# Kernel optimization log

Hardware: AMD Instinct MI355X
Metric: run time of the kernel (lower is better)

The kernel has to match this reference:

```python
import jax, jax.numpy as jnp
from jax import lax
import numpy as np

B, T, L, D, TOPK, KC = 8, 4096, 256, 128, 8, 9  # KC = ctx conv kernel size


def setup_inputs() -> dict:
    key = jax.random.key(0)
    ks = jax.random.split(key, 9)
    s = 0.05
    return {
        "x": jax.random.normal(ks[0], (B, T), jnp.float32),
        "lag_embed": jax.random.normal(ks[1], (L + 1, D), jnp.float32) * s,  # nn.Embedding(L+1, d)
        "val_w": jax.random.normal(ks[2], (D, 1), jnp.float32) * s,          # nn.Linear(1, d) weight
        "val_b": jnp.zeros((D,), jnp.float32),
        "conv_w": jax.random.normal(ks[3], (D, 1, KC), jnp.float32) * s,     # Conv1d(1, d, 9) weight (O,I,K)
        "conv_b": jnp.zeros((D,), jnp.float32),
        "ctx_w": jax.random.normal(ks[4], (D, D), jnp.float32) * s,          # ctx_proj
        "ctx_b": jnp.zeros((D,), jnp.float32),
        "wq": jax.random.normal(ks[5], (D, D), jnp.float32) * s,             # Wq (no bias)
        "wk": jax.random.normal(ks[6], (D, D), jnp.float32) * s,             # Wk (no bias)
        "bias_w": jax.random.normal(ks[7], (1, D), jnp.float32) * s,         # bias_head
        "bias_b": jnp.zeros((1,), jnp.float32),
    }


def _lag_bank(x, Lv):
    # Xlags[b, t, l] = x[b, t-(l+1)], left-padded with zeros (per docstring/intended math)
    Bv, Tv = x.shape
    pads = jnp.pad(x, ((0, 0), (Lv, 0)))
    idx = Lv - 1 + jnp.arange(Tv)[:, None] - jnp.arange(Lv)[None, :]  # (T, L)
    return pads[:, idx]  # (B, T, L)


def reference(x, lag_embed, val_w, val_b, conv_w, conv_b, ctx_w, ctx_b, wq, wk, bias_w, bias_b):
    Xlags = _lag_bank(x, L)  # (B, T, L)

    # Causal context conv: left-pad 8 zeros, Conv1d(1, D, 9, padding=0)
    xp = jnp.pad(x, ((0, 0), (KC - 1, 0)))[:, None, :]  # (B, 1, T+8)
    ctx = lax.conv_general_dilated(xp, conv_w, (1,), 'VALID',
                                   dimension_numbers=('NCH', 'OIH', 'NCH'))
    ctx = ctx + conv_b[None, :, None]           # (B, D, T)
    ctx = jnp.transpose(ctx, (0, 2, 1))         # (B, T, D)
    ctx = ctx @ ctx_w.T + ctx_b                 # ctx_proj

    q = ctx @ wq.T                              # (B, T, D)
    # score = <q, Wk Hlag> = <Wk^T q, Hlag>; Hlag = Xlags*val_w + (val_b + lag_embed[1:L+1])
    # is rank-1 in the value -> never materialize the (B,T,L,D) tensor.
    qk = q @ wk                                 # (B, T, D) = Wk^T q
    base = val_b[None, :] + lag_embed[1:L + 1]  # (L, D)
    logits = Xlags * (qk @ val_w[:, 0])[:, :, None] + qk @ base.T  # (B, T, L)

    # top-k sparsification (ties are measure-zero with continuous inputs)
    kth = lax.top_k(logits, TOPK)[0][..., -1:]
    masked = jnp.where(logits >= kth, logits, -jnp.inf)
    w = jax.nn.softmax(masked, axis=-1)         # (B, T, L)

    mu = jnp.sum(w * Xlags, axis=-1) + (ctx @ bias_w.T)[..., 0] + bias_b[0]  # (B, T)
    return mu, w
```

## Files before the change

kernel.cpp:

```cpp
#include <hip/hip_runtime.h>
#include <math.h>

#define D   128
#define LQ  256
#define KCQ 9
#define BQ  8
#define TQ  4096
#define RISK_DELTA 2e-5f
#define WCAP 16384

__global__ void pk1(const float* __restrict__ wk, const float* __restrict__ wq,
                    const float* __restrict__ ctx_w, const float* __restrict__ bias_w,
                    const float* __restrict__ conv_w, const float* __restrict__ val_b,
                    const float* __restrict__ lag_embed,
                    double* __restrict__ T2, double* __restrict__ u, int* __restrict__ wcnt,
                    float* __restrict__ ctx_wT, float* __restrict__ wqT,
                    float* __restrict__ conv_wT, float* __restrict__ baseT) {
    int tid = threadIdx.x;
    int bid = blockIdx.x;
    if (bid < D) {
        int d = bid;
        if (tid < D) {
            double acc = 0.0;
            for (int j = 0; j < D; ++j)
                acc += (double)wk[j * D + d] * (double)wq[j * D + tid];
            T2[d * D + tid] = acc;
            ctx_wT[d * D + tid] = ctx_w[tid * D + d];
            wqT[d * D + tid]    = wq[tid * D + d];
            if (d < KCQ) conv_wT[d * D + tid] = conv_w[tid * KCQ + d];
        }
        baseT[d * LQ + tid] = __fadd_rn(val_b[d], lag_embed[(size_t)(tid + 1) * D + d]);
    } else if (bid == D) {
        if (tid < D) {
            double acc = 0.0;
            for (int dd = 0; dd < D; ++dd)
                acc += (double)bias_w[dd] * (double)ctx_w[dd * D + tid];
            u[tid] = acc;
        }
    } else {
        if (tid == 0) *wcnt = 0;
    }
}

__global__ void pk2(const double* __restrict__ T2, const float* __restrict__ ctx_w,
                    const float* __restrict__ conv_w, const float* __restrict__ conv_b,
                    const float* __restrict__ ctx_b,
                    double* __restrict__ g, double* __restrict__ c1) {
    __shared__ double row[D];
    int d = blockIdx.x, e = threadIdx.x;
    double acc = 0.0;
    for (int j = 0; j < D; ++j)
        acc += T2[d * D + j] * (double)ctx_w[j * D + e];
    row[e] = acc;
    __syncthreads();
    if (e < KCQ) {
        double a = 0.0;
        for (int q = 0; q < D; ++q) a += row[q] * (double)conv_w[q * KCQ + e];
        g[e * D + d] = a;
    } else if (e == KCQ) {
        double a = 0.0;
        for (int q = 0; q < D; ++q) a += row[q] * (double)conv_b[q];
        for (int q = 0; q < D; ++q) a += T2[d * D + q] * (double)ctx_b[q];
        c1[d] = a;
    }
}

__global__ void pk3(const float* __restrict__ lag_embed, const float* __restrict__ val_b,
                    const float* __restrict__ val_w, const float* __restrict__ conv_w,
                    const float* __restrict__ conv_b, const float* __restrict__ ctx_b,
                    const float* __restrict__ bias_w, const float* __restrict__ bias_b,
                    const double* __restrict__ g, const double* __restrict__ c1,
                    const double* __restrict__ u,
                    double* __restrict__ gbT, double* __restrict__ cbv, double* __restrict__ cst) {
    int tid = threadIdx.x;
    if (blockIdx.x < LQ) {
        __shared__ double bl[D];
        int l = blockIdx.x;
        bl[tid] = (double)val_b[tid] + (double)lag_embed[(l + 1) * D + tid];
        __syncthreads();
        if (tid < KCQ) {
            double a = 0.0;
            for (int q = 0; q < D; ++q) a += bl[q] * g[tid * D + q];
            gbT[tid * LQ + l] = a;
        } else if (tid == KCQ) {
            double a = 0.0;
            for (int q = 0; q < D; ++q) a += bl[q] * c1[q];
            cbv[l] = a;
        }
    } else {
        if (tid < KCQ) {
            double a = 0.0, a2 = 0.0;
            for (int q = 0; q < D; ++q) a  += g[tid * D + q] * (double)val_w[q];
            for (int q = 0; q < D; ++q) a2 += u[q] * (double)conv_w[q * KCQ + tid];
            cst[tid]      = a;
            cst[10 + tid] = a2;
        } else if (tid == KCQ) {
            double a = 0.0, a2 = 0.0;
            for (int q = 0; q < D; ++q) a  += c1[q] * (double)val_w[q];
            for (int q = 0; q < D; ++q) a2 += u[q] * (double)conv_b[q];
            for (int q = 0; q < D; ++q) a2 += (double)bias_w[q] * (double)ctx_b[q];
            cst[9]  = a;
            cst[19] = a2 + (double)bias_b[0];
        }
    }
}

__global__ __launch_bounds__(256, 4) void lag_main(
    const float* __restrict__ x, const double* __restrict__ gbT,
    const double* __restrict__ cbv, const double* __restrict__ cst,
    float* __restrict__ muOut, float* __restrict__ wOut,
    int* __restrict__ wcnt, int* __restrict__ wlist) {
    __shared__ float sgb[KCQ * LQ];
    __shared__ float scb[LQ];
    __shared__ float sc[20];
    int tid = threadIdx.x;
    #pragma unroll
    for (int i = 0; i < KCQ; ++i) sgb[i * LQ + tid] = (float)gbT[i * LQ + tid];
    scb[tid] = (float)cbv[tid];
    if (tid < 20) sc[tid] = (float)cst[tid];
    __syncthreads();

    int wave = tid >> 6, lane = tid & 63;
    int row = blockIdx.x * 4 + wave;
    int b = row >> 12;
    int t = row & (TQ - 1);
    const float* xb = x + b * TQ;

    float xw[KCQ];
    #pragma unroll
    for (int k = 0; k < KCQ; ++k) {
        int idx = t - 8 + k;
        xw[k] = (idx >= 0) ? xb[idx] : 0.f;
    }
    float s = sc[9], bias = sc[19];
    #pragma unroll
    for (int k = 0; k < KCQ; ++k) {
        s    = fmaf(sc[k],      xw[k], s);
        bias = fmaf(sc[10 + k], xw[k], bias);
    }

    int l0 = lane * 4;
    float xlag[4];
    #pragma unroll
    for (int i = 0; i < 4; ++i) {
        int idx = t - 1 - (l0 + i);
        xlag[i] = (idx >= 0) ? xb[idx] : 0.f;
    }

    float4 cb4 = *reinterpret_cast<const float4*>(&scb[l0]);
    float lg[4] = {cb4.x, cb4.y, cb4.z, cb4.w};
    #pragma unroll
    for (int k = 0; k < KCQ; ++k) {
        float4 g4 = *reinterpret_cast<const float4*>(&sgb[k * LQ + l0]);
        lg[0] = fmaf(g4.x, xw[k], lg[0]);
        lg[1] = fmaf(g4.y, xw[k], lg[1]);
        lg[2] = fmaf(g4.z, xw[k], lg[2]);
        lg[3] = fmaf(g4.w, xw[k], lg[3]);
    }
    #pragma unroll
    for (int i = 0; i < 4; ++i) lg[i] = fmaf(xlag[i], s, lg[i]);

    const float NEG_INF = -__builtin_inff();
    float wl0 = lg[0], wl1 = lg[1], wl2 = lg[2], wl3 = lg[3];
    float mx = 0.f, thr = 0.f, v9 = 0.f;
    #pragma unroll
    for (int it = 0; it < 9; ++it) {
        float lm = fmaxf(fmaxf(wl0, wl1), fmaxf(wl2, wl3));
        float m = lm;
        #pragma unroll
        for (int off = 32; off >= 1; off >>= 1)
            m = fmaxf(m, __shfl_xor(m, off, 64));
        if (it == 0) mx = m;
        if (it == 7) thr = m;
        if (it == 8) v9 = m;
        if (it < 8) {
            unsigned long long ball = __ballot(lm == m);
            int leader = __ffsll(ball) - 1;
            if (lane == leader) {
                if (wl0 == m)      wl0 = NEG_INF;
                else if (wl1 == m) wl1 = NEG_INF;
                else if (wl2 == m) wl2 = NEG_INF;
                else               wl3 = NEG_INF;
            }
        }
    }

    if ((thr - v9) < RISK_DELTA) {
        if (lane == 0) {
            int pos = atomicAdd(wcnt, 1);
            if (pos < WCAP) wlist[pos] = row;
        }
        return;
    }

    float p[4], psum = 0.f, pmu = 0.f;
    #pragma unroll
    for (int j = 0; j < 4; ++j) {
        p[j] = (lg[j] >= thr) ? __expf(lg[j] - mx) : 0.f;
        psum += p[j];
        pmu = fmaf(p[j], xlag[j], pmu);
    }
    #pragma unroll
    for (int off = 32; off >= 1; off >>= 1) {
        psum += __shfl_xor(psum, off, 64);
        pmu  += __shfl_xor(pmu,  off, 64);
    }
    float inv = 1.f / psum;
    float4 wo = make_float4(p[0] * inv, p[1] * inv, p[2] * inv, p[3] * inv);
    *reinterpret_cast<float4*>(&wOut[(size_t)row * LQ + l0]) = wo;
    if (lane == 0) muOut[row] = fmaf(pmu, inv, bias);
}

__global__ __launch_bounds__(256) void fixer(
    const float* __restrict__ x, const float* __restrict__ wk,
    const float* __restrict__ val_w, const float* __restrict__ conv_b,
    const float* __restrict__ ctx_b, const float* __restrict__ bias_w,
    const float* __restrict__ bias_b,
    const float* __restrict__ ctx_wT, const float* __restrict__ wqT,
    const float* __restrict__ conv_wT, const float* __restrict__ baseT,
    const int* __restrict__ wcnt, const int* __restrict__ wlist,
    float* __restrict__ muOut, float* __restrict__ wOut) {
    __shared__ float sxw[8][KCQ];
    __shared__ float sctxc[8][D];
    __shared__ float sctxp[8][D];
    __shared__ float sq[8][D];
    __shared__ float sqk[8][D];
    __shared__ float ssv[8];
    __shared__ float sbd[8];
    __shared__ float slog[8][LQ];
    __shared__ int   srow[8];

    int cnt = *wcnt;
    if (cnt > WCAP) cnt = WCAP;
    int ngroups = (cnt + 7) >> 3;
    int tid = threadIdx.x;

    for (int gi = blockIdx.x; gi < ngroups; gi += gridDim.x) {
        if (tid < 8) {
            int idx = gi * 8 + tid;
            if (idx >= cnt) idx = cnt - 1;
            srow[tid] = wlist[idx];
        }
        __syncthreads();
        if (tid < 8 * KCQ) {
            int g = tid / KCQ, k = tid % KCQ;
            int row = srow[g]; int b = row >> 12, t = row & (TQ - 1);
            int ii = t - 8 + k;
            sxw[g][k] = (ii >= 0) ? x[b * TQ + ii] : 0.f;
        }
        __syncthreads();

        {
            int d = tid & (D - 1), gh = tid >> 7;
            float cw[KCQ];
            #pragma unroll
            for (int k = 0; k < KCQ; ++k) cw[k] = conv_wT[k * D + d];
            #pragma unroll 1
            for (int g = gh * 4; g < gh * 4 + 4; ++g) {
                float a = 0.f;
                #pragma unroll
                for (int k = 0; k < KCQ; ++k)
                    a = fmaf(cw[k], sxw[g][k], a);
                sctxc[g][d] = __fadd_rn(a, conv_b[d]);
            }
        }
        __syncthreads();

        {
            int e = tid & (D - 1), gh = tid >> 7, g0 = gh * 4;
            float a0 = 0.f, a1 = 0.f, a2 = 0.f, a3 = 0.f;
            float wv0[16], wv1[16];
            #pragma unroll
            for (int u = 0; u < 16; ++u) wv0[u] = ctx_wT[u * D + e];
            #pragma unroll 1
            for (int d2 = 0; d2 < D; d2 += 32) {
                #pragma unroll
                for (int u = 0; u < 16; ++u) wv1[u] = ctx_wT[(d2 + 16 + u) * D + e];
                #pragma unroll
                for (int u = 0; u < 16; ++u) {
                    a0 = fmaf(wv0[u], sctxc[g0 + 0][d2 + u], a0);
                    a1 = fmaf(wv0[u], sctxc[g0 + 1][d2 + u], a1);
                    a2 = fmaf(wv0[u], sctxc[g0 + 2][d2 + u], a2);
                    a3 = fmaf(wv0[u], sctxc[g0 + 3][d2 + u], a3);
                }
                if (d2 + 32 < D) {
                    #pragma unroll
                    for (int u = 0; u < 16; ++u) wv0[u] = ctx_wT[(d2 + 32 + u) * D + e];
                }
                #pragma unroll
                for (int u = 0; u < 16; ++u) {
                    a0 = fmaf(wv1[u], sctxc[g0 + 0][d2 + 16 + u], a0);
                    a1 = fmaf(wv1[u], sctxc[g0 + 1][d2 + 16 + u], a1);
                    a2 = fmaf(wv1[u], sctxc[g0 + 2][d2 + 16 + u], a2);
                    a3 = fmaf(wv1[u], sctxc[g0 + 3][d2 + 16 + u], a3);
                }
            }
            float cb = ctx_b[e];
            sctxp[g0 + 0][e] = __fadd_rn(a0, cb);
            sctxp[g0 + 1][e] = __fadd_rn(a1, cb);
            sctxp[g0 + 2][e] = __fadd_rn(a2, cb);
            sctxp[g0 + 3][e] = __fadd_rn(a3, cb);
        }
        __syncthreads();

        {
            int a = tid & (D - 1), gh = tid >> 7, g0 = gh * 4;
            float a0 = 0.f, a1 = 0.f, a2 = 0.f, a3 = 0.f;
            float wv0[16], wv1[16];
            #pragma unroll
            for (int u = 0; u < 16; ++u) wv0[u] = wqT[u * D + a];
            #pragma unroll 1
            for (int e2 = 0; e2 < D; e2 += 32) {
                #pragma unroll
                for (int u = 0; u < 16; ++u) wv1[u] = wqT[(e2 + 16 + u) * D + a];
                #pragma unroll
                for (int u = 0; u < 16; ++u) {
                    a0 = fmaf(wv0[u], sctxp[g0 + 0][e2 + u], a0);
                    a1 = fmaf(wv0[u], sctxp[g0 + 1][e2 + u], a1);
                    a2 = fmaf(wv0[u], sctxp[g0 + 2][e2 + u], a2);
                    a3 = fmaf(wv0[u], sctxp[g0 + 3][e2 + u], a3);
                }
                if (e2 + 32 < D) {
                    #pragma unroll
                    for (int u = 0; u < 16; ++u) wv0[u] = wqT[(e2 + 32 + u) * D + a];
                }
                #pragma unroll
                for (int u = 0; u < 16; ++u) {
                    a0 = fmaf(wv1[u], sctxp[g0 + 0][e2 + 16 + u], a0);
                    a1 = fmaf(wv1[u], sctxp[g0 + 1][e2 + 16 + u], a1);
                    a2 = fmaf(wv1[u], sctxp[g0 + 2][e2 + 16 + u], a2);
                    a3 = fmaf(wv1[u], sctxp[g0 + 3][e2 + 16 + u], a3);
                }
            }
            sq[g0 + 0][a] = a0;
            sq[g0 + 1][a] = a1;
            sq[g0 + 2][a] = a2;
            sq[g0 + 3][a] = a3;
        }
        __syncthreads();

        {
            int d = tid & (D - 1), gh = tid >> 7, g0 = gh * 4;
            float a0 = 0.f, a1 = 0.f, a2 = 0.f, a3 = 0.f;
            float wv0[16], wv1[16];
            #pragma unroll
            for (int u = 0; u < 16; ++u) wv0[u] = wk[u * D + d];
            #pragma unroll 1
            for (int a2i = 0; a2i < D; a2i += 32) {
                #pragma unroll
                for (int u = 0; u < 16; ++u) wv1[u] = wk[(a2i + 16 + u) * D + d];
                #pragma unroll
                for (int u = 0; u < 16; ++u) {
                    a0 = fmaf(wv0[u], sq[g0 + 0][a2i + u], a0);
                    a1 = fmaf(wv0[u], sq[g0 + 1][a2i + u], a1);
                    a2 = fmaf(wv0[u], sq[g0 + 2][a2i + u], a2);
                    a3 = fmaf(wv0[u], sq[g0 + 3][a2i + u], a3);
                }
                if (a2i + 32 < D) {
                    #pragma unroll
                    for (int u = 0; u < 16; ++u) wv0[u] = wk[(a2i + 32 + u) * D + d];
                }
                #pragma unroll
                for (int u = 0; u < 16; ++u) {
                    a0 = fmaf(wv1[u], sq[g0 + 0][a2i + 16 + u], a0);
                    a1 = fmaf(wv1[u], sq[g0 + 1][a2i + 16 + u], a1);
                    a2 = fmaf(wv1[u], sq[g0 + 2][a2i + 16 + u], a2);
                    a3 = fmaf(wv1[u], sq[g0 + 3][a2i + 16 + u], a3);
                }
            }
            sqk[g0 + 0][d] = a0;
            sqk[g0 + 1][d] = a1;
            sqk[g0 + 2][d] = a2;
            sqk[g0 + 3][d] = a3;
        }
        __syncthreads();

        if (tid < 8) {
            int g = tid;
            float a = 0.f;
            #pragma unroll 1
            for (int d2 = 0; d2 < D; d2 += 16) {
                float vv[16];
                #pragma unroll
                for (int u = 0; u < 16; ++u) vv[u] = val_w[d2 + u];
                #pragma unroll
                for (int u = 0; u < 16; ++u) a = fmaf(sqk[g][d2 + u], vv[u], a);
            }
            ssv[g] = a;
        } else if (tid < 16) {
            int g = tid - 8;
            float a = 0.f;
            #pragma unroll 1
            for (int e2 = 0; e2 < D; e2 += 16) {
                float vv[16];
                #pragma unroll
                for (int u = 0; u < 16; ++u) vv[u] = bias_w[e2 + u];
                #pragma unroll
                for (int u = 0; u < 16; ++u) a = fmaf(sctxp[g][e2 + u], vv[u], a);
            }
            sbd[g] = a;
        }
        __syncthreads();

        {
            int l = tid;
            float c0 = 0.f, c1a = 0.f, c2 = 0.f, c3 = 0.f, c4 = 0.f, c5 = 0.f, c6 = 0.f, c7 = 0.f;
            float bd0[16], bd1[16];
            #pragma unroll
            for (int u = 0; u < 16; ++u) bd0[u] = baseT[u * LQ + l];
            #pragma unroll 1
            for (int d2 = 0; d2 < D; d2 += 32) {
                #pragma unroll
                for (int u = 0; u < 16; ++u) bd1[u] = baseT[(d2 + 16 + u) * LQ + l];
                #pragma unroll
                for (int u = 0; u < 16; ++u) {
                    c0 = fmaf(bd0[u], sqk[0][d2 + u], c0);
                    c1a = fmaf(bd0[u], sqk[1][d2 + u], c1a);
                    c2 = fmaf(bd0[u], sqk[2][d2 + u], c2);
                    c3 = fmaf(bd0[u], sqk[3][d2 + u], c3);
                    c4 = fmaf(bd0[u], sqk[4][d2 + u], c4);
                    c5 = fmaf(bd0[u], sqk[5][d2 + u], c5);
                    c6 = fmaf(bd0[u], sqk[6][d2 + u], c6);
                    c7 = fmaf(bd0[u], sqk[7][d2 + u], c7);
                }
                if (d2 + 32 < D) {
                    #pragma unroll
                    for (int u = 0; u < 16; ++u) bd0[u] = baseT[(d2 + 32 + u) * LQ + l];
                }
                #pragma unroll
                for (int u = 0; u < 16; ++u) {
                    c0 = fmaf(bd1[u], sqk[0][d2 + 16 + u], c0);
                    c1a = fmaf(bd1[u], sqk[1][d2 + 16 + u], c1a);
                    c2 = fmaf(bd1[u], sqk[2][d2 + 16 + u], c2);
                    c3 = fmaf(bd1[u], sqk[3][d2 + 16 + u], c3);
                    c4 = fmaf(bd1[u], sqk[4][d2 + 16 + u], c4);
                    c5 = fmaf(bd1[u], sqk[5][d2 + 16 + u], c5);
                    c6 = fmaf(bd1[u], sqk[6][d2 + 16 + u], c6);
                    c7 = fmaf(bd1[u], sqk[7][d2 + 16 + u], c7);
                }
            }
            float accs[8] = {c0, c1a, c2, c3, c4, c5, c6, c7};
            #pragma unroll
            for (int g = 0; g < 8; ++g) {
                int row = srow[g]; int b = row >> 12, t = row & (TQ - 1);
                int ii = t - 1 - l;
                float xl = (ii >= 0) ? x[b * TQ + ii] : 0.f;
                slog[g][l] = __fadd_rn(__fmul_rn(xl, ssv[g]), accs[g]);
            }
        }
        __syncthreads();

        {
            int wave = tid >> 6, lane = tid & 63;
            #pragma unroll 1
            for (int gg = wave * 2; gg < wave * 2 + 2; ++gg) {
                float lv0 = slog[gg][lane], lv1 = slog[gg][lane + 64];
                float lv2 = slog[gg][lane + 128], lv3 = slog[gg][lane + 192];
                const float NEG_INF = -__builtin_inff();
                float w0 = lv0, w1 = lv1, w2 = lv2, w3 = lv3;
                float mx = 0.f, thr = 0.f;
                #pragma unroll
                for (int it = 0; it < 8; ++it) {
                    float lm = fmaxf(fmaxf(w0, w1), fmaxf(w2, w3));
                    float m = lm;
                    #pragma unroll
                    for (int off = 32; off >= 1; off >>= 1)
                        m = fmaxf(m, __shfl_xor(m, off, 64));
                    if (it == 0) mx = m;
                    thr = m;
                    if (it < 7) {
                        unsigned long long ball = __ballot(lm == m);
                        int leader = __ffsll(ball) - 1;
                        if (lane == leader) {
                            if (w0 == m)      w0 = NEG_INF;
                            else if (w1 == m) w1 = NEG_INF;
                            else if (w2 == m) w2 = NEG_INF;
                            else              w3 = NEG_INF;
                        }
                    }
                }
                int row = srow[gg]; int b = row >> 12, t = row & (TQ - 1);
                float p[4], xlg[4];
                double ps = 0.0;
                float lvs[4] = {lv0, lv1, lv2, lv3};
                #pragma unroll
                for (int j = 0; j < 4; ++j) {
                    int l = lane + 64 * j;
                    int ii = t - 1 - l;
                    xlg[j] = (ii >= 0) ? x[b * TQ + ii] : 0.f;
                    p[j] = (lvs[j] >= thr) ? (float)exp((double)__fsub_rn(lvs[j], mx)) : 0.f;
                    ps += (double)p[j];
                }
                #pragma unroll
                for (int off = 32; off >= 1; off >>= 1)
                    ps += __shfl_xor(ps, off, 64);
                float psf = (float)ps;
                double mud = 0.0;
                #pragma unroll
                for (int j = 0; j < 4; ++j) {
                    float wv = __fdiv_rn(p[j], psf);
                    wOut[(size_t)row * LQ + lane + 64 * j] = wv;
                    mud += (double)__fmul_rn(wv, xlg[j]);
                }
                #pragma unroll
                for (int off = 32; off >= 1; off >>= 1)
                    mud += __shfl_xor(mud, off, 64);
                if (lane == 0) {
                    float m1 = (float)mud;
                    m1 = __fadd_rn(m1, sbd[gg]);
                    m1 = __fadd_rn(m1, bias_b[0]);
                    muOut[row] = m1;
                }
            }
        }
        __syncthreads();
    }
}

extern "C" void kernel_launch(void* const* d_in, const int* in_sizes, int n_in,
                              void* d_out, int out_size, void* d_ws, size_t ws_size,
                              hipStream_t stream) {
    const float* x         = (const float*)d_in[0];
    const float* lag_embed = (const float*)d_in[1];
    const float* val_w     = (const float*)d_in[2];
    const float* val_b     = (const float*)d_in[3];
    const float* conv_w    = (const float*)d_in[4];
    const float* conv_b    = (const float*)d_in[5];
    const float* ctx_w     = (const float*)d_in[6];
    const float* ctx_b     = (const float*)d_in[7];
    const float* wq        = (const float*)d_in[8];
    const float* wk        = (const float*)d_in[9];
    const float* bias_w    = (const float*)d_in[10];
    const float* bias_b    = (const float*)d_in[11];

    char* wsb = (char*)d_ws;
    double* T2  = (double*)wsb;
    double* g   = T2 + 16384;
    double* u   = g + 1152;
    double* c1  = u + 128;
    double* gbT = c1 + 128;
    double* cbv = gbT + 2304;
    double* cst = cbv + 256;
    int* wcnt  = (int*)(wsb + 163840);
    int* wlist = wcnt + 1;
    float* ctx_wT  = (float*)(wsb + 229504);
    float* wqT     = ctx_wT + 16384;
    float* conv_wT = wqT + 16384;
    float* baseT   = conv_wT + 1152;

    float* muOut = (float*)d_out;
    float* wOut  = muOut + BQ * TQ;

    hipLaunchKernelGGL(pk1, dim3(D + 2), dim3(256), 0, stream,
                       wk, wq, ctx_w, bias_w, conv_w, val_b, lag_embed,
                       T2, u, wcnt, ctx_wT, wqT, conv_wT, baseT);
    hipLaunchKernelGGL(pk2, dim3(D), dim3(D), 0, stream, T2, ctx_w, conv_w, conv_b, ctx_b, g, c1);
    hipLaunchKernelGGL(pk3, dim3(LQ + 1), dim3(D), 0, stream,
                       lag_embed, val_b, val_w, conv_w, conv_b, ctx_b, bias_w, bias_b,
                       g, c1, u, gbT, cbv, cst);
    hipLaunchKernelGGL(lag_main, dim3(BQ * TQ / 4), dim3(256), 0, stream,
                       x, gbT, cbv, cst, muOut, wOut, wcnt, wlist);
    hipLaunchKernelGGL(fixer, dim3(256), dim3(256), 0, stream,
                       x, wk, val_w, conv_b, ctx_b, bias_w, bias_b,
                       ctx_wT, wqT, conv_wT, baseT, wcnt, wlist, muOut, wOut);
}
```

Before: 101.0 us.

## Store precomputed tables as float, raise occupancy, simplify top-k removal

The precompute kernel now writes its gbT/cbv/cst tables directly as float, so the main kernel no longer loads doubles and converts them when staging into shared memory. The main kernel's launch bounds rise from 4 to 8 blocks per SM to allow more concurrency. The top-k extraction loop replaces the ballot/leader single-element removal with a branch-free per-lane select. That select removes every element equal to the max, which differs from the old code only on exact ties. The fixer's bias dot product also drops its 16-wide register staging for a plain loop.

New measurement: 106.6 us. 5.5% more time.

```diff
diff --git a/kernel.cpp b/kernel.cpp
--- a/kernel.cpp
+++ b/kernel.cpp
@@ -71,7 +71,7 @@
                     const float* __restrict__ bias_w, const float* __restrict__ bias_b,
                     const double* __restrict__ g, const double* __restrict__ c1,
                     const double* __restrict__ u,
-                    double* __restrict__ gbT, double* __restrict__ cbv, double* __restrict__ cst) {
+                    float* __restrict__ gbTf, float* __restrict__ cbvf, float* __restrict__ cstf) {
     int tid = threadIdx.x;
     if (blockIdx.x < LQ) {
         __shared__ double bl[D];
@@ -81,33 +81,33 @@
         if (tid < KCQ) {
             double a = 0.0;
             for (int q = 0; q < D; ++q) a += bl[q] * g[tid * D + q];
-            gbT[tid * LQ + l] = a;
+            gbTf[tid * LQ + l] = (float)a;
         } else if (tid == KCQ) {
             double a = 0.0;
             for (int q = 0; q < D; ++q) a += bl[q] * c1[q];
-            cbv[l] = a;
+            cbvf[l] = (float)a;
         }
     } else {
         if (tid < KCQ) {
             double a = 0.0, a2 = 0.0;
             for (int q = 0; q < D; ++q) a  += g[tid * D + q] * (double)val_w[q];
             for (int q = 0; q < D; ++q) a2 += u[q] * (double)conv_w[q * KCQ + tid];
-            cst[tid]      = a;
-            cst[10 + tid] = a2;
+            cstf[tid]      = (float)a;
+            cstf[10 + tid] = (float)a2;
         } else if (tid == KCQ) {
             double a = 0.0, a2 = 0.0;
             for (int q = 0; q < D; ++q) a  += c1[q] * (double)val_w[q];
             for (int q = 0; q < D; ++q) a2 += u[q] * (double)conv_b[q];
             for (int q = 0; q < D; ++q) a2 += (double)bias_w[q] * (double)ctx_b[q];
-            cst[9]  = a;
-            cst[19] = a2 + (double)bias_b[0];
+            cstf[9]  = (float)a;
+            cstf[19] = (float)(a2 + (double)bias_b[0]);
         }
     }
 }
 
-__global__ __launch_bounds__(256, 4) void lag_main(
-    const float* __restrict__ x, const double* __restrict__ gbT,
-    const double* __restrict__ cbv, const double* __restrict__ cst,
+__global__ __launch_bounds__(256, 8) void lag_main(
+    const float* __restrict__ x, const float* __restrict__ gbTf,
+    const float* __restrict__ cbvf, const float* __restrict__ cstf,
     float* __restrict__ muOut, float* __restrict__ wOut,
     int* __restrict__ wcnt, int* __restrict__ wlist) {
     __shared__ float sgb[KCQ * LQ];
@@ -115,9 +115,9 @@
     __shared__ float sc[20];
     int tid = threadIdx.x;
     #pragma unroll
-    for (int i = 0; i < KCQ; ++i) sgb[i * LQ + tid] = (float)gbT[i * LQ + tid];
-    scb[tid] = (float)cbv[tid];
-    if (tid < 20) sc[tid] = (float)cst[tid];
+    for (int i = 0; i < KCQ; ++i) sgb[i * LQ + tid] = gbTf[i * LQ + tid];
+    scb[tid] = cbvf[tid];
+    if (tid < 20) sc[tid] = cstf[tid];
     __syncthreads();
 
     int wave = tid >> 6, lane = tid & 63;
@@ -174,14 +174,10 @@
         if (it == 7) thr = m;
         if (it == 8) v9 = m;
         if (it < 8) {
-            unsigned long long ball = __ballot(lm == m);
-            int leader = __ffsll(ball) - 1;
-            if (lane == leader) {
-                if (wl0 == m)      wl0 = NEG_INF;
-                else if (wl1 == m) wl1 = NEG_INF;
-                else if (wl2 == m) wl2 = NEG_INF;
-                else               wl3 = NEG_INF;
-            }
+            wl0 = (wl0 == m) ? NEG_INF : wl0;
+            wl1 = (wl1 == m) ? NEG_INF : wl1;
+            wl2 = (wl2 == m) ? NEG_INF : wl2;
+            wl3 = (wl3 == m) ? NEG_INF : wl3;
         }
     }
 
@@ -391,12 +387,8 @@
             int g = tid - 8;
             float a = 0.f;
             #pragma unroll 1
-            for (int e2 = 0; e2 < D; e2 += 16) {
-                float vv[16];
-                #pragma unroll
-                for (int u = 0; u < 16; ++u) vv[u] = bias_w[e2 + u];
-                #pragma unroll
-                for (int u = 0; u < 16; ++u) a = fmaf(sctxp[g][e2 + u], vv[u], a);
+            for (int e2 = 0; e2 < D; ++e2) {
+                a = fmaf(sctxp[g][e2], bias_w[e2], a);
             }
             sbd[g] = a;
         }
@@ -538,9 +530,9 @@
     double* g   = T2 + 16384;
     double* u   = g + 1152;
     double* c1  = u + 128;
-    double* gbT = c1 + 128;
-    double* cbv = gbT + 2304;
-    double* cst = cbv + 256;
+    float* gbTf = (float*)(c1 + 128);
+    float* cbvf = gbTf + 2304;
+    float* cstf = cbvf + 256;
     int* wcnt  = (int*)(wsb + 163840);
     int* wlist = wcnt + 1;
     float* ctx_wT  = (float*)(wsb + 229504);
@@ -557,9 +549,9 @@
     hipLaunchKernelGGL(pk2, dim3(D), dim3(D), 0, stream, T2, ctx_w, conv_w, conv_b, ctx_b, g, c1);
     hipLaunchKernelGGL(pk3, dim3(LQ + 1), dim3(D), 0, stream,
                        lag_embed, val_b, val_w, conv_w, conv_b, ctx_b, bias_w, bias_b,
-                       g, c1, u, gbT, cbv, cst);
+                       g, c1, u, gbTf, cbvf, cstf);
     hipLaunchKernelGGL(lag_main, dim3(BQ * TQ / 4), dim3(256), 0, stream,
-                       x, gbT, cbv, cst, muOut, wOut, wcnt, wlist);
+                       x, gbTf, cbvf, cstf, muOut, wOut, wcnt, wlist);
     hipLaunchKernelGGL(fixer, dim3(256), dim3(256), 0, stream,
                        x, wk, val_w, conv_b, ctx_b, bias_w, bias_b,
                        ctx_wT, wqT, conv_wT, baseT, wcnt, wlist, muOut, wOut);
```
